# Kernel tuning notes

Hardware: AMD Instinct MI355X
Metric: run time of the kernel (lower is better)

The kernel has to match this reference:

```python
import jax, jax.numpy as jnp
import numpy as np

B, T, C = 4, 2048, 1024
H = 16
D = C // H  # head_size = 64


def setup_inputs() -> dict:
    key = jax.random.key(0)
    ks = jax.random.split(key, 9)
    s = 1.0 / np.sqrt(C)  # keep activations well-scaled
    return {
        "x": jax.random.normal(ks[0], (B, T, C), dtype=jnp.float32),
        "Wq": jax.random.normal(ks[1], (C, C), dtype=jnp.float32) * s,
        "bq": jnp.zeros((C,), dtype=jnp.float32),
        "Wk": jax.random.normal(ks[2], (C, C), dtype=jnp.float32) * s,
        "bk": jnp.zeros((C,), dtype=jnp.float32),
        "Wv": jax.random.normal(ks[3], (C, C), dtype=jnp.float32) * s,
        "bv": jnp.zeros((C,), dtype=jnp.float32),
        "Wp": jax.random.normal(ks[4], (C, C), dtype=jnp.float32) * s,
        "bp": jnp.zeros((C,), dtype=jnp.float32),
    }


def reference(x, Wq, bq, Wk, bk, Wv, bv, Wp, bp):
    # QKV projections: [B,T,C] -> [B,H,T,D]
    def heads(y):
        return y.reshape(B, T, H, D).transpose(0, 2, 1, 3)

    q = heads(x @ Wq + bq)
    k = heads(x @ Wk + bk)
    v = heads(x @ Wv + bv)

    # scaled dot-product attention scores [B,H,T,T]
    attn = jnp.einsum("bhqd,bhkd->bhqk", q, k) * (D ** -0.5)
    causal = jnp.tril(jnp.ones((T, T), dtype=bool))  # [T,T]
    attn = jnp.where(causal[None, None, :, :], attn, -jnp.inf)
    attn = jax.nn.softmax(attn, axis=-1)
    # dropout = 0.0 -> identity

    y = jnp.einsum("bhqk,bhkd->bhqd", attn, v)  # [B,H,T,D]
    y = y.transpose(0, 2, 1, 3).reshape(B, T, C)
    return y @ Wp + bp
```

## Files before the change

kernel.cpp:

```cpp
#include <hip/hip_runtime.h>
#include <math.h>

static constexpr int Bsz = 4;
static constexpr int Tn  = 2048;
static constexpr int Cn  = 1024;
static constexpr int Hn  = 16;
static constexpr int Dn  = 64;

typedef __attribute__((ext_vector_type(8))) short bf16x8;
typedef __attribute__((ext_vector_type(4))) float f32x4;

#define MFMA16(a, b, c) __builtin_amdgcn_mfma_f32_16x16x32_bf16((a), (b), (c), 0, 0, 0)

static constexpr float kQScale = 0.18033688f;
static constexpr float kFixedM = 24.0f;

__device__ __forceinline__ unsigned short f2bf(float f) {
  unsigned u = __float_as_uint(f);
  unsigned r = (u + 0x7fffu + ((u >> 16) & 1u)) >> 16;
  return (unsigned short)r;
}

__device__ __forceinline__ unsigned cvtpk_bf16(float lo, float hi) {
  unsigned r;
  asm("v_cvt_pk_bf16_f32 %0, %1, %2" : "=v"(r) : "v"(lo), "v"(hi));
  return r;
}

__device__ __forceinline__ void load_lds16(const void* g, void* l) {
  __builtin_amdgcn_global_load_lds(
      (const __attribute__((address_space(1))) void*)g,
      (__attribute__((address_space(3))) void*)l, 16, 0, 0);
}

__global__ __launch_bounds__(256) void convert_x_k(
    const float* __restrict__ x, unsigned short* __restrict__ xb) {
  const int i = blockIdx.x * blockDim.x + threadIdx.x;
  const float4 a = ((const float4*)x)[i * 2 + 0];
  const float4 b = ((const float4*)x)[i * 2 + 1];
  uint4 o;
  o.x = cvtpk_bf16(a.x, a.y);
  o.y = cvtpk_bf16(a.z, a.w);
  o.z = cvtpk_bf16(b.x, b.y);
  o.w = cvtpk_bf16(b.z, b.w);
  ((uint4*)xb)[i] = o;
}

__global__ __launch_bounds__(256) void transpose_w_k(
    const float* __restrict__ w0, const float* __restrict__ w1,
    const float* __restrict__ w2, const float* __restrict__ w3,
    unsigned short* __restrict__ o0, unsigned short* __restrict__ o1,
    unsigned short* __restrict__ o2, unsigned short* __restrict__ o3) {
  __shared__ unsigned short Ts[64][65];
  const float* W;
  unsigned short* O;
  switch (blockIdx.z) {
    case 0: W = w0; O = o0; break;
    case 1: W = w1; O = o1; break;
    case 2: W = w2; O = o2; break;
    default: W = w3; O = o3; break;
  }
  const int k0 = blockIdx.y * 64, n0 = blockIdx.x * 64;
  const int tid = threadIdx.x;
  const int cr = tid >> 4, cc = (tid & 15) * 4;
#pragma unroll
  for (int p = 0; p < 4; ++p) {
    const int r = p * 16 + cr;
    const float4 v = *(const float4*)&W[(size_t)(k0 + r) * Cn + n0 + cc];
    Ts[r][cc + 0] = f2bf(v.x);
    Ts[r][cc + 1] = f2bf(v.y);
    Ts[r][cc + 2] = f2bf(v.z);
    Ts[r][cc + 3] = f2bf(v.w);
  }
  __syncthreads();
#pragma unroll
  for (int p = 0; p < 4; ++p) {
    const int n = p * 16 + cr;
    ushort4 o;
    o.x = Ts[cc + 0][n];
    o.y = Ts[cc + 1][n];
    o.z = Ts[cc + 2][n];
    o.w = Ts[cc + 3][n];
    *(ushort4*)&O[(size_t)(n0 + n) * Cn + k0 + cc] = o;
  }
}

__device__ __forceinline__ void gemm_core(
    const unsigned short* __restrict__ A, const unsigned short* __restrict__ Bt,
    int row0, int col0, unsigned short* As, unsigned short* Bs,
    f32x4 acc[4][4]) {
  const int tid = threadIdx.x;
  const int lane = tid & 63, w = tid >> 6;
  const int wm = w >> 1, wn = w & 1;
  const int lr = lane & 15, lg = lane >> 4;

  auto stage = [&](int buf, int k0) {
#pragma unroll
    for (int it = 0; it < 4; ++it) {
      const int c = it * 256 + tid;
      const int r = c >> 3;
      const int lc = (c & 7) ^ (r & 7);
      load_lds16(A + (size_t)(row0 + r) * Cn + k0 + lc * 8,
                 &As[buf * 8192 + c * 8]);
    }
#pragma unroll
    for (int it = 0; it < 4; ++it) {
      const int c = it * 256 + tid;
      const int r = c >> 3;
      const int lc = (c & 7) ^ (r & 7);
      load_lds16(Bt + (size_t)(col0 + r) * Cn + k0 + lc * 8,
                 &Bs[buf * 8192 + c * 8]);
    }
  };

  stage(0, 0);
  for (int ki = 0; ki < 16; ++ki) {
    const int cur = ki & 1;
    const bool pf = (ki < 15);
    if (pf) stage(cur ^ 1, (ki + 1) * 64);
    if (pf) asm volatile("s_waitcnt vmcnt(8)" ::: "memory");
    else    asm volatile("s_waitcnt vmcnt(0)" ::: "memory");
    __builtin_amdgcn_s_barrier();
#pragma unroll
    for (int ks = 0; ks < 2; ++ks) {
      bf16x8 af[4], bfr[4];
#pragma unroll
      for (int mi = 0; mi < 4; ++mi)
        af[mi] = *(const bf16x8*)
            &As[cur * 8192 + (wm * 64 + mi * 16 + lr) * 64 +
                (((ks * 4 + lg) ^ (lr & 7)) << 3)];
#pragma unroll
      for (int ni = 0; ni < 4; ++ni)
        bfr[ni] = *(const bf16x8*)
            &Bs[cur * 8192 + (wn * 64 + ni * 16 + lr) * 64 +
                (((ks * 4 + lg) ^ (lr & 7)) << 3)];
#pragma unroll
      for (int mi = 0; mi < 4; ++mi)
#pragma unroll
        for (int ni = 0; ni < 4; ++ni)
          acc[mi][ni] = MFMA16(af[mi], bfr[ni], acc[mi][ni]);
    }
    if (pf) __builtin_amdgcn_s_barrier();
  }
}

__global__ __launch_bounds__(256, 2) void qkv_gemm_k(
    const unsigned short* __restrict__ A,
    const unsigned short* __restrict__ Wq, const unsigned short* __restrict__ Wk,
    const unsigned short* __restrict__ Wv,
    const float* __restrict__ bq, const float* __restrict__ bk,
    const float* __restrict__ bv,
    unsigned short* __restrict__ Qo, unsigned short* __restrict__ Ko,
    unsigned short* __restrict__ Vo) {
  __shared__ unsigned short As[2 * 128 * 64];
  __shared__ unsigned short Bs[2 * 128 * 64];
  const int z = blockIdx.z;
  const unsigned short* Bt = (z == 0) ? Wq : (z == 1) ? Wk : Wv;
  const float* bias = (z == 0) ? bq : (z == 1) ? bk : bv;
  unsigned short* out = (z == 0) ? Qo : (z == 1) ? Ko : Vo;
  const float scale = (z == 0) ? kQScale : 1.0f;

  const int row0 = blockIdx.x * 128, col0 = blockIdx.y * 128;
  const f32x4 fz = {0.f, 0.f, 0.f, 0.f};
  f32x4 acc[4][4];
#pragma unroll
  for (int i = 0; i < 4; ++i)
#pragma unroll
    for (int j = 0; j < 4; ++j) acc[i][j] = fz;

  gemm_core(A, Bt, row0, col0, As, Bs, acc);

  const int lane = threadIdx.x & 63, w = threadIdx.x >> 6;
  const int wm = w >> 1, wn = w & 1;
  const int lr = lane & 15, lg = lane >> 4;
#pragma unroll
  for (int mi = 0; mi < 4; ++mi) {
#pragma unroll
    for (int ni = 0; ni < 4; ++ni) {
      const int col = col0 + wn * 64 + ni * 16 + lr;
      const float bv_ = bias[col];
      const int h = col >> 6, d = col & 63;
      const int rbase = row0 + wm * 64 + mi * 16 + lg * 4;
      const int b = rbase >> 11, t0 = rbase & (Tn - 1);
      if (z == 2) {
        ushort4 o4;
        o4.x = f2bf(acc[mi][ni][0] + bv_);
        o4.y = f2bf(acc[mi][ni][1] + bv_);
        o4.z = f2bf(acc[mi][ni][2] + bv_);
        o4.w = f2bf(acc[mi][ni][3] + bv_);
        *(ushort4*)&out[(((size_t)b * Hn + h) * Dn + d) * Tn + t0] = o4;
      } else {
#pragma unroll
        for (int r = 0; r < 4; ++r) {
          const float val = (acc[mi][ni][r] + bv_) * scale;
          out[((((size_t)b * Hn + h) * Tn + (t0 + r)) << 6) + d] = f2bf(val);
        }
      }
    }
  }
}

__global__ __launch_bounds__(256, 2) void proj_gemm_k(
    const unsigned short* __restrict__ A, const unsigned short* __restrict__ Bt,
    const float* __restrict__ bias, float* __restrict__ out) {
  __shared__ unsigned short As[2 * 128 * 64];
  __shared__ unsigned short Bs[2 * 128 * 64];
  const int row0 = blockIdx.x * 128, col0 = blockIdx.y * 128;
  const f32x4 fz = {0.f, 0.f, 0.f, 0.f};
  f32x4 acc[4][4];
#pragma unroll
  for (int i = 0; i < 4; ++i)
#pragma unroll
    for (int j = 0; j < 4; ++j) acc[i][j] = fz;

  gemm_core(A, Bt, row0, col0, As, Bs, acc);

  const int lane = threadIdx.x & 63, w = threadIdx.x >> 6;
  const int wm = w >> 1, wn = w & 1;
  const int lr = lane & 15, lg = lane >> 4;
#pragma unroll
  for (int mi = 0; mi < 4; ++mi) {
#pragma unroll
    for (int ni = 0; ni < 4; ++ni) {
      const int col = col0 + wn * 64 + ni * 16 + lr;
      const float bv_ = bias[col];
#pragma unroll
      for (int r = 0; r < 4; ++r) {
        const int row = row0 + wm * 64 + mi * 16 + lg * 4 + r;
        out[(size_t)row * Cn + col] = acc[mi][ni][r] + bv_;
      }
    }
  }
}

__global__ __launch_bounds__(256, 4) void attn_mfma_k(
    const unsigned short* __restrict__ Q, const unsigned short* __restrict__ K,
    const unsigned short* __restrict__ Vt, unsigned short* __restrict__ Y) {
  __shared__ unsigned short Ks[2][64 * 64];
  __shared__ unsigned short Vs[2][64 * 64];
  __shared__ unsigned short Ps[4][16 * 64];
  const int tid = threadIdx.x, lane = tid & 63, w = tid >> 6;
  const int lr = lane & 15, lg = lane >> 4;
  const int bh = blockIdx.x;
  const int qt = (int)gridDim.y - 1 - blockIdx.y;
  const size_t base = (size_t)bh * Tn * Dn;

  bf16x8 qf[2];
  const int qrow = qt * 64 + w * 16 + lr;
#pragma unroll
  for (int ks = 0; ks < 2; ++ks)
    qf[ks] = *(const bf16x8*)&Q[base + (size_t)qrow * Dn + ks * 32 + lg * 8];

  auto stage_K = [&](int buf, int kt) {
#pragma unroll
    for (int it = 0; it < 2; ++it) {
      const int c = it * 256 + tid;
      const int r = c >> 3;
      const int lc = (c & 7) ^ (r & 7);
      load_lds16(K + base + (size_t)(kt * 64 + r) * Dn + lc * 8, &Ks[buf][c * 8]);
    }
  };
  auto stage_V = [&](int buf, int kt) {
#pragma unroll
    for (int it = 0; it < 2; ++it) {
      const int c = it * 256 + tid;
      const int r = c >> 3;
      const int lc = (c & 7) ^ (r & 7);
      load_lds16(Vt + base + (size_t)r * Tn + kt * 64 + lc * 8, &Vs[buf][c * 8]);
    }
  };

  const f32x4 fz = {0.f, 0.f, 0.f, 0.f};
  f32x4 oacc[4];
#pragma unroll
  for (int i = 0; i < 4; ++i) oacc[i] = fz;
  float l_run = 0.f;

  stage_K(0, 0);
  stage_V(0, 0);
  asm volatile("s_waitcnt vmcnt(2)" ::: "memory");
  __builtin_amdgcn_s_barrier();

  for (int kt = 0; kt <= qt; ++kt) {
    const int cur = kt & 1;
    const bool pf = (kt < qt);
    if (pf) {
      stage_K(cur ^ 1, kt + 1);
      stage_V(cur ^ 1, kt + 1);
    }

    f32x4 s[4];
#pragma unroll
    for (int ni = 0; ni < 4; ++ni) s[ni] = fz;
    __builtin_amdgcn_s_setprio(1);
#pragma unroll
    for (int ni = 0; ni < 4; ++ni)
#pragma unroll
      for (int ks = 0; ks < 2; ++ks) {
        const bf16x8 kf = *(const bf16x8*)
            &Ks[cur][(ni * 16 + lr) * 64 + (((ks * 4 + lg) ^ (lr & 7)) << 3)];
        s[ni] = MFMA16(kf, qf[ks], s[ni]);
      }
    __builtin_amdgcn_s_setprio(0);

    const bool diag = (kt == qt);
    uint2 pw[4];
#pragma unroll
    for (int ni = 0; ni < 4; ++ni) {
      float p[4];
#pragma unroll
      for (int r = 0; r < 4; ++r) {
        float v = s[ni][r];
        if (diag) {
          const int gk = kt * 64 + ni * 16 + lg * 4 + r;
          if (gk > qrow) v = -1e30f;
        }
        p[r] = exp2f(v - kFixedM);
      }
      l_run += (p[0] + p[1]) + (p[2] + p[3]);
      pw[ni].x = cvtpk_bf16(p[0], p[1]);
      pw[ni].y = cvtpk_bf16(p[2], p[3]);
    }

#pragma unroll
    for (int ni = 0; ni < 4; ++ni) {
      const int byte = lr * 128 + ((((ni * 2) + (lg >> 1)) ^ (lr & 7)) << 4) +
                       ((lg & 1) << 3);
      *(uint2*)((char*)&Ps[w][0] + byte) = pw[ni];
    }

    if (pf) {
      asm volatile("s_waitcnt vmcnt(4)" ::: "memory");
    } else {
      asm volatile("s_waitcnt vmcnt(0)" ::: "memory");
    }
    __builtin_amdgcn_s_barrier();

    __builtin_amdgcn_s_setprio(1);
#pragma unroll
    for (int ks = 0; ks < 2; ++ks) {
      const bf16x8 pa = *(const bf16x8*)
          &Ps[w][lr * 64 + (((ks * 4 + lg) ^ (lr & 7)) << 3)];
#pragma unroll
      for (int nd = 0; nd < 4; ++nd) {
        const bf16x8 vf = *(const bf16x8*)
            &Vs[cur][(nd * 16 + lr) * 64 + (((ks * 4 + lg) ^ (lr & 7)) << 3)];
        oacc[nd] = MFMA16(pa, vf, oacc[nd]);
      }
    }
    __builtin_amdgcn_s_setprio(0);

    if (pf) {
      asm volatile("s_waitcnt vmcnt(2)" ::: "memory");
      __builtin_amdgcn_s_barrier();
    }
  }

  l_run += __shfl_xor(l_run, 16);
  l_run += __shfl_xor(l_run, 32);

  const int b = bh >> 4, h = bh & 15;
#pragma unroll
  for (int i = 0; i < 4; ++i) {
    const float li = __shfl(l_run, lg * 4 + i);
    const float inv = 1.f / li;
    const int t = qt * 64 + w * 16 + lg * 4 + i;
#pragma unroll
    for (int nd = 0; nd < 4; ++nd) {
      const int d = nd * 16 + lr;
      Y[((size_t)b * Tn + t) * Cn + h * Dn + d] = f2bf(oacc[nd][i] * inv);
    }
  }
}

extern "C" void kernel_launch(void* const* d_in, const int* in_sizes, int n_in,
                              void* d_out, int out_size, void* d_ws, size_t ws_size,
                              hipStream_t stream) {
  const float* x  = (const float*)d_in[0];
  const float* Wq = (const float*)d_in[1];
  const float* bq = (const float*)d_in[2];
  const float* Wk = (const float*)d_in[3];
  const float* bk = (const float*)d_in[4];
  const float* Wv = (const float*)d_in[5];
  const float* bv = (const float*)d_in[6];
  const float* Wp = (const float*)d_in[7];
  const float* bp = (const float*)d_in[8];
  float* out = (float*)d_out;

  const size_t xe = (size_t)Bsz * Tn * Cn;
  const size_t we = (size_t)Cn * Cn;
  unsigned short* p = (unsigned short*)d_ws;
  unsigned short* xb  = p; p += xe;
  unsigned short* Wqt = p; p += we;
  unsigned short* Wkt = p; p += we;
  unsigned short* Wvt = p; p += we;
  unsigned short* Wpt = p; p += we;
  unsigned short* Qb  = p; p += xe;
  unsigned short* Kb  = p; p += xe;
  unsigned short* Vtb = p; p += xe;
  unsigned short* Yb  = p; p += xe;

  convert_x_k<<<dim3((int)(xe / 8 / 256)), dim3(256), 0, stream>>>(x, xb);
  transpose_w_k<<<dim3(16, 16, 4), dim3(256), 0, stream>>>(
      Wq, Wk, Wv, Wp, Wqt, Wkt, Wvt, Wpt);

  qkv_gemm_k<<<dim3((Bsz * Tn) / 128, Cn / 128, 3), dim3(256), 0, stream>>>(
      xb, Wqt, Wkt, Wvt, bq, bk, bv, Qb, Kb, Vtb);

  attn_mfma_k<<<dim3(Bsz * Hn, Tn / 64), dim3(256), 0, stream>>>(Qb, Kb, Vtb, Yb);

  proj_gemm_k<<<dim3((Bsz * Tn) / 128, Cn / 128), dim3(256), 0, stream>>>(
      Yb, Wpt, bp, out);
}
```

Measured before the change: 164.7 us.

## Fuse Q/K/V projections into one kernel sharing the A tile

Replaces the three-way z-dimension QKV GEMM launch with one kernel that keeps three accumulator sets and stages the x tile once per K-step alongside three weight tiles. This removes repeated global and LDS loading of the activation tile across the three projections. The K-step is halved to 32 to fit LDS, and MFMA sections are wrapped in s_setprio. Accumulator registers triple, which risks spills or reduced occupancy, and the grid shrinks threefold.

```diff
diff --git a/kernel.cpp b/kernel.cpp
--- a/kernel.cpp
+++ b/kernel.cpp
@@ -144,7 +144,7 @@
   }
 }
 
-__global__ __launch_bounds__(256, 2) void qkv_gemm_k(
+__global__ __launch_bounds__(256, 2) void qkv_fused_k(
     const unsigned short* __restrict__ A,
     const unsigned short* __restrict__ Wq, const unsigned short* __restrict__ Wk,
     const unsigned short* __restrict__ Wv,
@@ -152,49 +152,133 @@
     const float* __restrict__ bv,
     unsigned short* __restrict__ Qo, unsigned short* __restrict__ Ko,
     unsigned short* __restrict__ Vo) {
-  __shared__ unsigned short As[2 * 128 * 64];
-  __shared__ unsigned short Bs[2 * 128 * 64];
-  const int z = blockIdx.z;
-  const unsigned short* Bt = (z == 0) ? Wq : (z == 1) ? Wk : Wv;
-  const float* bias = (z == 0) ? bq : (z == 1) ? bk : bv;
-  unsigned short* out = (z == 0) ? Qo : (z == 1) ? Ko : Vo;
-  const float scale = (z == 0) ? kQScale : 1.0f;
-
-  const int row0 = blockIdx.x * 128, col0 = blockIdx.y * 128;
-  const f32x4 fz = {0.f, 0.f, 0.f, 0.f};
-  f32x4 acc[4][4];
-#pragma unroll
-  for (int i = 0; i < 4; ++i)
-#pragma unroll
-    for (int j = 0; j < 4; ++j) acc[i][j] = fz;
-
-  gemm_core(A, Bt, row0, col0, As, Bs, acc);
-
-  const int lane = threadIdx.x & 63, w = threadIdx.x >> 6;
+  __shared__ unsigned short As[2][128 * 32];
+  __shared__ unsigned short Bs[2][3][128 * 32];
+  const int tid = threadIdx.x, lane = tid & 63, w = tid >> 6;
   const int wm = w >> 1, wn = w & 1;
   const int lr = lane & 15, lg = lane >> 4;
+  const int row0 = blockIdx.x * 128, col0 = blockIdx.y * 128;
+
+  auto stage = [&](int buf, int k0) {
+    const unsigned short* Ws[3] = {Wq, Wk, Wv};
+#pragma unroll
+    for (int it = 0; it < 2; ++it) {
+      const int c = it * 256 + tid;
+      const int r = c >> 2;
+      const int lc = (c & 3) ^ ((r >> 1) & 3);
+      load_lds16(A + (size_t)(row0 + r) * Cn + k0 + lc * 8, &As[buf][c * 8]);
+    }
+#pragma unroll
+    for (int z = 0; z < 3; ++z)
+#pragma unroll
+      for (int it = 0; it < 2; ++it) {
+        const int c = it * 256 + tid;
+        const int r = c >> 2;
+        const int lc = (c & 3) ^ ((r >> 1) & 3);
+        load_lds16(Ws[z] + (size_t)(col0 + r) * Cn + k0 + lc * 8,
+                   &Bs[buf][z][c * 8]);
+      }
+  };
+
+  const f32x4 fz = {0.f, 0.f, 0.f, 0.f};
+  f32x4 acc0[4][4], acc1[4][4], acc2[4][4];
+#pragma unroll
+  for (int i = 0; i < 4; ++i)
+#pragma unroll
+    for (int j = 0; j < 4; ++j) { acc0[i][j] = fz; acc1[i][j] = fz; acc2[i][j] = fz; }
+
+  stage(0, 0);
+  for (int ki = 0; ki < 32; ++ki) {
+    const int cur = ki & 1;
+    const bool pf = (ki < 31);
+    if (pf) stage(cur ^ 1, (ki + 1) * 32);
+    if (pf) asm volatile("s_waitcnt vmcnt(8)" ::: "memory");
+    else    asm volatile("s_waitcnt vmcnt(0)" ::: "memory");
+    __builtin_amdgcn_s_barrier();
+
+    const int kchunk = (lg ^ ((lr >> 1) & 3)) << 3;
+    bf16x8 af[4];
+#pragma unroll
+    for (int mi = 0; mi < 4; ++mi)
+      af[mi] = *(const bf16x8*)
+          &As[cur][(wm * 64 + mi * 16 + lr) * 32 + kchunk];
+
+    {
+      bf16x8 bfr[4];
+#pragma unroll
+      for (int ni = 0; ni < 4; ++ni)
+        bfr[ni] = *(const bf16x8*)
+            &Bs[cur][0][(wn * 64 + ni * 16 + lr) * 32 + kchunk];
+      __builtin_amdgcn_s_setprio(1);
+#pragma unroll
+      for (int mi = 0; mi < 4; ++mi)
+#pragma unroll
+        for (int ni = 0; ni < 4; ++ni)
+          acc0[mi][ni] = MFMA16(af[mi], bfr[ni], acc0[mi][ni]);
+      __builtin_amdgcn_s_setprio(0);
+    }
+    {
+      bf16x8 bfr[4];
+#pragma unroll
+      for (int ni = 0; ni < 4; ++ni)
+        bfr[ni] = *(const bf16x8*)
+            &Bs[cur][1][(wn * 64 + ni * 16 + lr) * 32 + kchunk];
+      __builtin_amdgcn_s_setprio(1);
+#pragma unroll
+      for (int mi = 0; mi < 4; ++mi)
+#pragma unroll
+        for (int ni = 0; ni < 4; ++ni)
+          acc1[mi][ni] = MFMA16(af[mi], bfr[ni], acc1[mi][ni]);
+      __builtin_amdgcn_s_setprio(0);
+    }
+    {
+      bf16x8 bfr[4];
+#pragma unroll
+      for (int ni = 0; ni < 4; ++ni)
+        bfr[ni] = *(const bf16x8*)
+            &Bs[cur][2][(wn * 64 + ni * 16 + lr) * 32 + kchunk];
+      __builtin_amdgcn_s_setprio(1);
+#pragma unroll
+      for (int mi = 0; mi < 4; ++mi)
+#pragma unroll
+        for (int ni = 0; ni < 4; ++ni)
+          acc2[mi][ni] = MFMA16(af[mi], bfr[ni], acc2[mi][ni]);
+      __builtin_amdgcn_s_setprio(0);
+    }
+
+    if (pf) __builtin_amdgcn_s_barrier();
+  }
+
 #pragma unroll
   for (int mi = 0; mi < 4; ++mi) {
 #pragma unroll
     for (int ni = 0; ni < 4; ++ni) {
       const int col = col0 + wn * 64 + ni * 16 + lr;
-      const float bv_ = bias[col];
       const int h = col >> 6, d = col & 63;
       const int rbase = row0 + wm * 64 + mi * 16 + lg * 4;
       const int b = rbase >> 11, t0 = rbase & (Tn - 1);
-      if (z == 2) {
+      {
+        const float bv_ = bq[col];
+#pragma unroll
+        for (int r = 0; r < 4; ++r)
+          Qo[((((size_t)b * Hn + h) * Tn + (t0 + r)) << 6) + d] =
+              f2bf((acc0[mi][ni][r] + bv_) * kQScale);
+      }
+      {
+        const float bv_ = bk[col];
+#pragma unroll
+        for (int r = 0; r < 4; ++r)
+          Ko[((((size_t)b * Hn + h) * Tn + (t0 + r)) << 6) + d] =
+              f2bf(acc1[mi][ni][r] + bv_);
+      }
+      {
+        const float bv_ = bv[col];
         ushort4 o4;
-        o4.x = f2bf(acc[mi][ni][0] + bv_);
-        o4.y = f2bf(acc[mi][ni][1] + bv_);
-        o4.z = f2bf(acc[mi][ni][2] + bv_);
-        o4.w = f2bf(acc[mi][ni][3] + bv_);
-        *(ushort4*)&out[(((size_t)b * Hn + h) * Dn + d) * Tn + t0] = o4;
-      } else {
-#pragma unroll
-        for (int r = 0; r < 4; ++r) {
-          const float val = (acc[mi][ni][r] + bv_) * scale;
-          out[((((size_t)b * Hn + h) * Tn + (t0 + r)) << 6) + d] = f2bf(val);
-        }
+        o4.x = f2bf(acc2[mi][ni][0] + bv_);
+        o4.y = f2bf(acc2[mi][ni][1] + bv_);
+        o4.z = f2bf(acc2[mi][ni][2] + bv_);
+        o4.w = f2bf(acc2[mi][ni][3] + bv_);
+        *(ushort4*)&Vo[(((size_t)b * Hn + h) * Dn + d) * Tn + t0] = o4;
       }
     }
   }
@@ -404,7 +488,7 @@
   transpose_w_k<<<dim3(16, 16, 4), dim3(256), 0, stream>>>(
       Wq, Wk, Wv, Wp, Wqt, Wkt, Wvt, Wpt);
 
-  qkv_gemm_k<<<dim3((Bsz * Tn) / 128, Cn / 128, 3), dim3(256), 0, stream>>>(
+  qkv_fused_k<<<dim3((Bsz * Tn) / 128, Cn / 128), dim3(256), 0, stream>>>(
       xb, Wqt, Wkt, Wvt, bq, bk, bv, Qb, Kb, Vtb);
 
   attn_mfma_k<<<dim3(Bsz * Hn, Tn / 64), dim3(256), 0, stream>>>(Qb, Kb, Vtb, Yb);
```

Result: faster. 160.3 us (-2.7%).
